# Optimization experiments

Hardware: AMD Instinct MI355X
Metric: run time of the kernel (lower is better)

## Reference

```python
import jax, jax.numpy as jnp
import numpy as np


def setup_inputs() -> dict:
    key = jax.random.key(0)
    ks = jax.random.split(key, 7)
    B, N, D, F, E = 4, 2048, 1024, 4096, 8
    s_in = 1.0 / np.sqrt(D)
    s_ff = 1.0 / np.sqrt(F)
    return {
        "x": jax.random.normal(ks[0], (B, N, D), dtype=jnp.float32),
        "Wg": jax.random.normal(ks[1], (D, E), dtype=jnp.float32) * s_in,
        "bg": jnp.zeros((E,), dtype=jnp.float32),
        "W1": jax.random.normal(ks[2], (E, D, F), dtype=jnp.float32) * s_in,
        "b1": jnp.zeros((E, F), dtype=jnp.float32),
        "W2": jax.random.normal(ks[3], (E, F, D), dtype=jnp.float32) * s_ff,
        "b2": jnp.zeros((E, D), dtype=jnp.float32),
    }


def reference(x, Wg, bg, W1, b1, W2, b2):
    TOP_K = 2
    # Gating: softmax over experts, then top-k (dropout is inference no-op)
    gate_scores = jax.nn.softmax(x @ Wg + bg, axis=-1)          # [B,N,E]
    topk_scores, topk_idx = jax.lax.top_k(gate_scores, TOP_K)   # [B,N,K]

    # Dense all-expert FFN (matches reference: every expert on every token)
    h = jax.nn.relu(jnp.einsum("bnd,edf->ebnf", x, W1) + b1[:, None, None, :])
    eo = jnp.einsum("ebnf,efd->ebnd", h, W2) + b2[:, None, None, :]  # [E,B,N,D]

    # Gather top-k expert outputs per token and combine
    eo_bne = jnp.transpose(eo, (1, 2, 0, 3))                     # [B,N,E,D]
    gathered = jnp.take_along_axis(eo_bne, topk_idx[..., None], axis=2)  # [B,N,K,D]
    output = jnp.sum(topk_scores[..., None] * gathered, axis=2)  # [B,N,D]
    return output
```

## Files before the change

kernel.cpp:

```cpp
#include <hip/hip_runtime.h>
#include <stdint.h>


#define E_ 8
#define D_ 1024
#define F_ 4096
#define NTOK 8192

typedef __bf16 bf16x8 __attribute__((ext_vector_type(8)));
typedef float f32x4 __attribute__((ext_vector_type(4)));
typedef unsigned short ushort_t;

__device__ __forceinline__ ushort_t f2bf(float f) {
  union { float f; unsigned u; } v; v.f = f;
  unsigned r = v.u + 0x7fff + ((v.u >> 16) & 1);
  return (ushort_t)(r >> 16);
}

__device__ __forceinline__ void gload16(const void* g, void* l) {
  __builtin_amdgcn_global_load_lds((__attribute__((address_space(1))) void*)(g),
                                   (__attribute__((address_space(3))) void*)(l),
                                   16, 0, 0);
}

__global__ __launch_bounds__(256) void gate_k(const float* __restrict__ x,
    const float* __restrict__ Wg, const float* __restrict__ bg,
    int* counts, int* tk_idx, float* tk_score) {
  __shared__ float wg[E_ * D_];
  for (int i = threadIdx.x; i < D_ * E_; i += 256) wg[(i & 7) * D_ + (i >> 3)] = Wg[i];
  __syncthreads();
  const int lane = threadIdx.x & 63;
  const int wv = threadIdx.x >> 6;
  const int t = blockIdx.x * 4 + wv;
  const float* xr = x + (size_t)t * D_;
  double acc[E_];
#pragma unroll
  for (int e = 0; e < E_; ++e) acc[e] = 0.0;
  for (int i = 0; i < D_ / 64; ++i) {
    const int d = i * 64 + lane;
    const double xv = (double)xr[d];
#pragma unroll
    for (int e = 0; e < E_; ++e) acc[e] += xv * (double)wg[e * D_ + d];
  }
#pragma unroll
  for (int e = 0; e < E_; ++e) {
    double v = acc[e];
#pragma unroll
    for (int s = 32; s > 0; s >>= 1) v += __shfl_xor(v, s, 64);
    acc[e] = v;
  }
  if (lane == 0) {
    double l[E_], m = -1e300;
#pragma unroll
    for (int e = 0; e < E_; ++e) { l[e] = acc[e] + (double)bg[e]; m = (l[e] > m) ? l[e] : m; }
    double p[E_], s = 0.0;
#pragma unroll
    for (int e = 0; e < E_; ++e) { p[e] = exp(l[e] - m); s += p[e]; }
    int i1 = 0;
#pragma unroll
    for (int e = 1; e < E_; ++e) if (p[e] > p[i1]) i1 = e;
    int i2 = -1;
#pragma unroll
    for (int e = 0; e < E_; ++e) if (e != i1 && (i2 < 0 || p[e] > p[i2])) i2 = e;
    tk_idx[2 * t] = i1; tk_idx[2 * t + 1] = i2;
    tk_score[2 * t] = (float)(p[i1] / s);
    tk_score[2 * t + 1] = (float)(p[i2] / s);
    atomicAdd(&counts[i1], 1);
    atomicAdd(&counts[i2], 1);
  }
}

__global__ void offsets_k(const int* __restrict__ counts, int* __restrict__ offsets) {
  if (threadIdx.x == 0) {
    int s = 0;
    for (int e = 0; e < E_; ++e) { offsets[e] = s; s += counts[e]; }
    offsets[E_] = s;
  }
}

__global__ __launch_bounds__(256) void assign_k(const int* __restrict__ tk_idx,
    const float* __restrict__ tk_score, const int* __restrict__ offsets,
    int* counts2, int* slot_token, float* slot_scale) {
  const int t = blockIdx.x * 256 + threadIdx.x;
#pragma unroll
  for (int k = 0; k < 2; ++k) {
    const int e = tk_idx[2 * t + k];
    const int pos = atomicAdd(&counts2[e], 1);
    const int slot = offsets[e] + pos;
    slot_token[slot] = t;
    slot_scale[slot] = tk_score[2 * t + k];
  }
}

__global__ __launch_bounds__(256) void convert_x_k(const float* __restrict__ x,
                                                   ushort_t* __restrict__ xb) {
  const size_t i = ((size_t)blockIdx.x * 256 + threadIdx.x) * 8;
  const float4 a = *(const float4*)(x + i);
  const float4 b = *(const float4*)(x + i + 4);
  union { ushort_t u[8]; uint4 v; } p;
  p.u[0] = f2bf(a.x); p.u[1] = f2bf(a.y); p.u[2] = f2bf(a.z); p.u[3] = f2bf(a.w);
  p.u[4] = f2bf(b.x); p.u[5] = f2bf(b.y); p.u[6] = f2bf(b.z); p.u[7] = f2bf(b.w);
  *(uint4*)(xb + i) = p.v;
}

__global__ __launch_bounds__(256) void transpose_conv(const float* __restrict__ in,
    ushort_t* __restrict__ out, int R, int C) {
  __shared__ float t[64][65];
  const int ex = blockIdx.z;
  const int c0 = blockIdx.x * 64, r0 = blockIdx.y * 64;
  const float* ein = in + (size_t)ex * R * C;
  ushort_t* eout = out + (size_t)ex * R * C;
  const int tid = threadIdx.x;
#pragma unroll
  for (int it = 0; it < 4; ++it) {
    const int idx = it * 256 + tid;
    const int r = idx >> 4, cv = (idx & 15) * 4;
    const float4 v = *(const float4*)(ein + (size_t)(r0 + r) * C + c0 + cv);
    t[cv + 0][r] = v.x; t[cv + 1][r] = v.y; t[cv + 2][r] = v.z; t[cv + 3][r] = v.w;
  }
  __syncthreads();
#pragma unroll
  for (int it = 0; it < 2; ++it) {
    const int idx = it * 256 + tid;
    const int c = idx >> 3, sg = (idx & 7) * 8;
    union { ushort_t u[8]; uint4 v; } p;
#pragma unroll
    for (int k = 0; k < 8; ++k) p.u[k] = f2bf(t[c][sg + k]);
    *(uint4*)(eout + (size_t)(c0 + c) * R + r0 + sg) = p.v;
  }
}

template <int MODE>
__global__ __launch_bounds__(512, 2) void moe_gemm(
    const ushort_t* __restrict__ A, const ushort_t* __restrict__ Bt,
    const float* __restrict__ bias,
    const int* __restrict__ offs, const int* __restrict__ counts,
    const int* __restrict__ slot_token, const float* __restrict__ slot_scale,
    ushort_t* __restrict__ H, float* __restrict__ Out, int N, int K) {
  const int e = blockIdx.z;
  const int cnt = counts[e];
  const int mb = blockIdx.y;
  if (mb * 256 >= cnt) return;
  const int off = offs[e];
  const int n0 = blockIdx.x * 256;

  extern __shared__ char smem[];

  const int tid = threadIdx.x;
  const int w = tid >> 6, l = tid & 63;
  const int wm = w >> 2, wn = w & 3;

  const int lr = l >> 3;
  const int swk = ((l & 7) * 16) ^ (lr << 4);
  const char* asrc[4];
  const char* bsrc[4];
#pragma unroll
  for (int q = 0; q < 4; ++q) {
    const int row = (w * 4 + q) * 8 + lr;
    int gm = mb * 256 + row;
    if (gm >= cnt) gm = cnt - 1;
    size_t arow;
    if (MODE == 0) arow = (size_t)slot_token[off + gm];
    else           arow = (size_t)(off + gm);
    asrc[q] = (const char*)A + arow * (size_t)K * 2 + swk;
    bsrc[q] = (const char*)Bt + ((size_t)e * N + (size_t)(n0 + row)) * (size_t)K * 2 + swk;
  }

  const int fr = l & 15, kg = l >> 4, rg = kg;
  const int sw = (fr & 7) << 4;
  const int baseA0 = (wm * 128 + fr) * 128 + ((kg * 16) ^ sw);
  const int baseA1 = (wm * 128 + fr) * 128 + ((64 + kg * 16) ^ sw);
  const int baseB0 = 32768 + (wn * 64 + fr) * 128 + ((kg * 16) ^ sw);
  const int baseB1 = 32768 + (wn * 64 + fr) * 128 + ((64 + kg * 16) ^ sw);

  f32x4 acc[8][4];
#pragma unroll
  for (int i = 0; i < 8; ++i)
#pragma unroll
    for (int j = 0; j < 4; ++j) { acc[i][j][0] = 0.f; acc[i][j][1] = 0.f; acc[i][j][2] = 0.f; acc[i][j][3] = 0.f; }

  const int nk = K / 64;
  int curOff = 0;

#define STAGE(KOFF, LOFF)                                                     \
  do {                                                                        \
    _Pragma("unroll")                                                         \
    for (int q = 0; q < 4; ++q)                                               \
      gload16(asrc[q] + (KOFF), smem + (LOFF) + (w * 4 + q) * 1024);          \
    _Pragma("unroll")                                                         \
    for (int q = 0; q < 4; ++q)                                               \
      gload16(bsrc[q] + (KOFF), smem + (LOFF) + 32768 + (w * 4 + q) * 1024);  \
  } while (0)

  STAGE(0, 0);
  __syncthreads();

  for (int kt = 0; kt < nk; ++kt) {
    if (kt + 1 < nk) STAGE((kt + 1) * 128, curOff ^ 65536);
#pragma unroll
    for (int s = 0; s < 2; ++s) {
      bf16x8 a[8], b[4];
      const int bA = curOff + (s ? baseA1 : baseA0);
      const int bB = curOff + (s ? baseB1 : baseB0);
#pragma unroll
      for (int i = 0; i < 8; ++i) a[i] = *(const bf16x8*)(smem + bA + i * 2048);
#pragma unroll
      for (int j = 0; j < 4; ++j) b[j] = *(const bf16x8*)(smem + bB + j * 2048);
#pragma unroll
      for (int i = 0; i < 8; ++i)
#pragma unroll
        for (int j = 0; j < 4; ++j)
          acc[i][j] = __builtin_amdgcn_mfma_f32_16x16x32_bf16(a[i], b[j], acc[i][j], 0, 0, 0);
    }
    __syncthreads();
    curOff ^= 65536;
  }
#undef STAGE

  const float* bias_e = bias + (size_t)e * N + n0;
#pragma unroll
  for (int i = 0; i < 8; ++i) {
#pragma unroll
    for (int q = 0; q < 4; ++q) {
      const int m = wm * 128 + i * 16 + rg * 4 + q;
      const int gm = mb * 256 + m;
      if (gm < cnt) {
        if (MODE == 0) {
          ushort_t* hr = H + (size_t)(off + gm) * (size_t)N + n0;
#pragma unroll
          for (int j = 0; j < 4; ++j) {
            const int n = wn * 64 + j * 16 + fr;
            float v = acc[i][j][q] + bias_e[n];
            hr[n] = f2bf(v > 0.f ? v : 0.f);
          }
        } else {
          const int slot = off + gm;
          const int tok = slot_token[slot];
          const float sc = slot_scale[slot];
          float* orow = Out + (size_t)tok * D_ + n0;
#pragma unroll
          for (int j = 0; j < 4; ++j) {
            const int n = wn * 64 + j * 16 + fr;
            float v = acc[i][j][q] + bias_e[n];
            atomicAdd(orow + n, sc * v);
          }
        }
      }
    }
  }
}

extern "C" void kernel_launch(void* const* d_in, const int* in_sizes, int n_in,
                              void* d_out, int out_size, void* d_ws, size_t ws_size,
                              hipStream_t stream) {
  const float* x  = (const float*)d_in[0];
  const float* Wg = (const float*)d_in[1];
  const float* bg = (const float*)d_in[2];
  const float* W1 = (const float*)d_in[3];
  const float* b1 = (const float*)d_in[4];
  const float* W2 = (const float*)d_in[5];
  const float* b2 = (const float*)d_in[6];
  float* out = (float*)d_out;
  char* ws = (char*)d_ws;

  int*   counts     = (int*)(ws + 0);
  int*   counts2    = (int*)(ws + 64);
  int*   offsets    = (int*)(ws + 128);
  int*   tk_idx     = (int*)(ws + 256);
  float* tk_score   = (float*)(ws + 256 + 65536);
  int*   slot_token = (int*)(ws + 256 + 2 * 65536);
  float* slot_scale = (float*)(ws + 256 + 3 * 65536);

  ushort_t* xb  = (ushort_t*)(ws + (1 << 20));
  ushort_t* w1t = xb + (size_t)NTOK * D_;
  ushort_t* w2t = w1t + (size_t)E_ * F_ * D_;
  ushort_t* h   = w2t + (size_t)E_ * D_ * F_;

  (void)hipFuncSetAttribute((const void*)moe_gemm<0>,
                            hipFuncAttributeMaxDynamicSharedMemorySize, 131072);
  (void)hipFuncSetAttribute((const void*)moe_gemm<1>,
                            hipFuncAttributeMaxDynamicSharedMemorySize, 131072);

  hipMemsetAsync(ws, 0, 256, stream);
  hipMemsetAsync(d_out, 0, sizeof(float) * (size_t)out_size, stream);

  convert_x_k<<<(NTOK * D_) / (256 * 8), 256, 0, stream>>>(x, xb);
  transpose_conv<<<dim3(F_ / 64, D_ / 64, E_), 256, 0, stream>>>(W1, w1t, D_, F_);
  transpose_conv<<<dim3(D_ / 64, F_ / 64, E_), 256, 0, stream>>>(W2, w2t, F_, D_);
  gate_k<<<NTOK / 4, 256, 0, stream>>>(x, Wg, bg, counts, tk_idx, tk_score);
  offsets_k<<<1, 64, 0, stream>>>(counts, offsets);
  assign_k<<<NTOK / 256, 256, 0, stream>>>(tk_idx, tk_score, offsets, counts2, slot_token, slot_scale);

  moe_gemm<0><<<dim3(F_ / 256, 64, E_), 512, 131072, stream>>>(
      xb, w1t, b1, offsets, counts, slot_token, slot_scale, h, nullptr, F_, D_);
  moe_gemm<1><<<dim3(D_ / 256, 64, E_), 512, 131072, stream>>>(
      h, w2t, b2, offsets, counts, slot_token, slot_scale, nullptr, out, D_, F_);
}
```

Baseline: 1.082 ms.

## Split K-tile into half-stages with 8-phase interleaved load/MFMA pipeline

After: 1.088 ms. About the same (+0.5%).

```diff
diff --git a/kernel.cpp b/kernel.cpp
--- a/kernel.cpp
+++ b/kernel.cpp
@@ -150,28 +150,29 @@
   const int w = tid >> 6, l = tid & 63;
   const int wm = w >> 2, wn = w & 3;
 
-  const int lr = l >> 3;
-  const int swk = ((l & 7) * 16) ^ (lr << 4);
-  const char* asrc[4];
-  const char* bsrc[4];
-#pragma unroll
-  for (int q = 0; q < 4; ++q) {
-    const int row = (w * 4 + q) * 8 + lr;
+  const int lr = l >> 2;
+  const int c16 = ((l & 3) ^ ((l >> 3) & 3)) << 4;
+  const char* aSrc[2];
+  const char* bSrc[2];
+#pragma unroll
+  for (int q = 0; q < 2; ++q) {
+    const int row = w * 32 + q * 16 + lr;
     int gm = mb * 256 + row;
     if (gm >= cnt) gm = cnt - 1;
     size_t arow;
     if (MODE == 0) arow = (size_t)slot_token[off + gm];
     else           arow = (size_t)(off + gm);
-    asrc[q] = (const char*)A + arow * (size_t)K * 2 + swk;
-    bsrc[q] = (const char*)Bt + ((size_t)e * N + (size_t)(n0 + row)) * (size_t)K * 2 + swk;
-  }
-
-  const int fr = l & 15, kg = l >> 4, rg = kg;
-  const int sw = (fr & 7) << 4;
-  const int baseA0 = (wm * 128 + fr) * 128 + ((kg * 16) ^ sw);
-  const int baseA1 = (wm * 128 + fr) * 128 + ((64 + kg * 16) ^ sw);
-  const int baseB0 = 32768 + (wn * 64 + fr) * 128 + ((kg * 16) ^ sw);
-  const int baseB1 = 32768 + (wn * 64 + fr) * 128 + ((64 + kg * 16) ^ sw);
+    aSrc[q] = (const char*)A + arow * (size_t)K * 2 + c16;
+    bSrc[q] = (const char*)Bt + ((size_t)e * N + (size_t)(n0 + row)) * (size_t)K * 2 + c16;
+  }
+
+  const int fr = l & 15, kg = l >> 4;
+  const int kb = ((kg ^ ((fr >> 1) & 3)) << 4);
+  int aoff[8], boff[4];
+#pragma unroll
+  for (int i = 0; i < 8; ++i) aoff[i] = (wm * 128 + i * 16 + fr) * 64 + kb;
+#pragma unroll
+  for (int j = 0; j < 4; ++j) boff[j] = (wn * 64 + j * 16 + fr) * 64 + kb;
 
   f32x4 acc[8][4];
 #pragma unroll
@@ -179,44 +180,77 @@
 #pragma unroll
     for (int j = 0; j < 4; ++j) { acc[i][j][0] = 0.f; acc[i][j][1] = 0.f; acc[i][j][2] = 0.f; acc[i][j][3] = 0.f; }
 
+#define STG_A(T, S, BUF)                                                              \
+  do {                                                                                \
+    gload16(aSrc[0] + (T) * 128 + (S) * 64,                                           \
+            smem + (BUF) * 65536 + (S) * 16384 + w * 2048);                           \
+    gload16(aSrc[1] + (T) * 128 + (S) * 64,                                           \
+            smem + (BUF) * 65536 + (S) * 16384 + w * 2048 + 1024);                    \
+  } while (0)
+#define STG_B(T, S, BUF)                                                              \
+  do {                                                                                \
+    gload16(bSrc[0] + (T) * 128 + (S) * 64,                                           \
+            smem + (BUF) * 65536 + 32768 + (S) * 16384 + w * 2048);                   \
+    gload16(bSrc[1] + (T) * 128 + (S) * 64,                                           \
+            smem + (BUF) * 65536 + 32768 + (S) * 16384 + w * 2048 + 1024);            \
+  } while (0)
+#define VM4 asm volatile("s_waitcnt vmcnt(4)" ::: "memory")
+
+#define PHASE(BUFR, IH, S, LOADB, STG, VM)                                            \
+  {                                                                                   \
+    bf16x8 a_[4];                                                                     \
+    const char* Ab = smem + (BUFR) * 65536 + (S) * 16384;                             \
+    _Pragma("unroll")                                                                 \
+    for (int ii = 0; ii < 4; ++ii) a_[ii] = *(const bf16x8*)(Ab + aoff[(IH) * 4 + ii]); \
+    if (LOADB) {                                                                      \
+      const char* Bb = Ab + 32768;                                                    \
+      _Pragma("unroll")                                                               \
+      for (int j = 0; j < 4; ++j) bfr[j] = *(const bf16x8*)(Bb + boff[j]);            \
+    }                                                                                 \
+    STG;                                                                              \
+    VM;                                                                               \
+    __builtin_amdgcn_s_barrier();                                                     \
+    asm volatile("s_waitcnt lgkmcnt(0)" ::: "memory");                                \
+    __builtin_amdgcn_sched_barrier(0);                                                \
+    __builtin_amdgcn_s_setprio(1);                                                    \
+    _Pragma("unroll")                                                                 \
+    for (int ii = 0; ii < 4; ++ii)                                                    \
+      _Pragma("unroll")                                                               \
+      for (int j = 0; j < 4; ++j)                                                     \
+        acc[(IH) * 4 + ii][j] = __builtin_amdgcn_mfma_f32_16x16x32_bf16(              \
+            a_[ii], bfr[j], acc[(IH) * 4 + ii][j], 0, 0, 0);                          \
+    __builtin_amdgcn_s_setprio(0);                                                    \
+    __builtin_amdgcn_sched_barrier(0);                                                \
+    __builtin_amdgcn_s_barrier();                                                     \
+  }
+
   const int nk = K / 64;
-  int curOff = 0;
-
-#define STAGE(KOFF, LOFF)                                                     \
-  do {                                                                        \
-    _Pragma("unroll")                                                         \
-    for (int q = 0; q < 4; ++q)                                               \
-      gload16(asrc[q] + (KOFF), smem + (LOFF) + (w * 4 + q) * 1024);          \
-    _Pragma("unroll")                                                         \
-    for (int q = 0; q < 4; ++q)                                               \
-      gload16(bsrc[q] + (KOFF), smem + (LOFF) + 32768 + (w * 4 + q) * 1024);  \
-  } while (0)
-
-  STAGE(0, 0);
-  __syncthreads();
-
-  for (int kt = 0; kt < nk; ++kt) {
-    if (kt + 1 < nk) STAGE((kt + 1) * 128, curOff ^ 65536);
-#pragma unroll
-    for (int s = 0; s < 2; ++s) {
-      bf16x8 a[8], b[4];
-      const int bA = curOff + (s ? baseA1 : baseA0);
-      const int bB = curOff + (s ? baseB1 : baseB0);
-#pragma unroll
-      for (int i = 0; i < 8; ++i) a[i] = *(const bf16x8*)(smem + bA + i * 2048);
-#pragma unroll
-      for (int j = 0; j < 4; ++j) b[j] = *(const bf16x8*)(smem + bB + j * 2048);
-#pragma unroll
-      for (int i = 0; i < 8; ++i)
-#pragma unroll
-        for (int j = 0; j < 4; ++j)
-          acc[i][j] = __builtin_amdgcn_mfma_f32_16x16x32_bf16(a[i], b[j], acc[i][j], 0, 0, 0);
-    }
-    __syncthreads();
-    curOff ^= 65536;
-  }
-#undef STAGE
-
+
+  STG_A(0, 0, 0); STG_B(0, 0, 0); STG_A(0, 1, 0); STG_B(0, 1, 0);
+  STG_A(1, 0, 1); STG_B(1, 0, 1);
+  VM4;
+  __builtin_amdgcn_s_barrier();
+
+  bf16x8 bfr[4];
+  for (int it = 0; it < nk / 2; ++it) {
+    const int tU = 2 * it + 1;
+    const int tV = (2 * it + 2 < nk) ? 2 * it + 2 : nk - 1;
+    const int tW = (2 * it + 3 < nk) ? 2 * it + 3 : nk - 1;
+    PHASE(0, 0, 0, 1, STG_A(tU, 1, 1), (void)0);
+    PHASE(0, 1, 0, 0, STG_B(tU, 1, 1), (void)0);
+    PHASE(0, 0, 1, 1, STG_A(tV, 0, 0), (void)0);
+    PHASE(0, 1, 1, 0, STG_B(tV, 0, 0), VM4);
+    PHASE(1, 0, 0, 1, STG_A(tV, 1, 0), (void)0);
+    PHASE(1, 1, 0, 0, STG_B(tV, 1, 0), (void)0);
+    PHASE(1, 0, 1, 1, STG_A(tW, 0, 1), (void)0);
+    PHASE(1, 1, 1, 0, STG_B(tW, 0, 1), VM4);
+  }
+#undef PHASE
+#undef STG_A
+#undef STG_B
+#undef VM4
+
+  const int rg = kg;
   const float* bias_e = bias + (size_t)e * N + n0;
 #pragma unroll
   for (int i = 0; i < 8; ++i) {
```
